# Kernel optimization log

Hardware: AMD Instinct MI355X
Metric: run time of the kernel (lower is better)

## Reference

```python
import jax, jax.numpy as jnp
import numpy as np

WEIGHT_GRADIENT = 0.05
EPS = 1e-6


def _normalize(q, eps):
    # torch F.normalize: q / max(||q||, eps)
    n = jnp.sqrt(jnp.sum(q * q, axis=1, keepdims=True))
    return q / jnp.maximum(n, eps)


def _grad_mag(q, eps):
    # depthwise conv with [-1,1] kernels == finite differences, then replicate-pad
    gx = q[..., :, 1:] - q[..., :, :-1]          # (B,4,H,W-1)
    gy = q[..., 1:, :] - q[..., :-1, :]          # (B,4,H-1,W)
    gx = jnp.pad(gx, ((0, 0), (0, 0), (0, 0), (0, 1)), mode='edge')
    gy = jnp.pad(gy, ((0, 0), (0, 0), (0, 1), (0, 0)), mode='edge')
    return jnp.sqrt(gx * gx + gy * gy + eps)


def setup_inputs() -> dict:
    key = jax.random.key(0)
    k1, k2, k3 = jax.random.split(key, 3)
    B, H, W, S = 16, 256, 256, 24
    q_pred = jax.random.normal(k1, (B, 4, H, W), dtype=jnp.float32)
    q_target = jax.random.normal(k2, (B, 4, H, W), dtype=jnp.float32)
    syms = jax.random.normal(k3, (S, 4), dtype=jnp.float32)
    syms = syms / jnp.linalg.norm(syms, axis=1, keepdims=True)  # unit quaternions
    return {"q_pred": q_pred, "q_target": q_target, "syms": syms}


def reference(q_pred, q_target, syms, eps=EPS):
    # (B,4,H,W) -> (N,4)
    qp = _normalize(q_pred.transpose(0, 2, 3, 1).reshape(-1, 4), eps)
    qt = _normalize(q_target.transpose(0, 2, 3, 1).reshape(-1, 4), eps)
    w1, x1, y1, z1 = qp[:, 0], qp[:, 1], qp[:, 2], qp[:, 3]
    w2, x2, y2, z2 = qt[:, 0], qt[:, 1], qt[:, 2], qt[:, 3]
    # relative quaternion r = qt * conj(qp)
    rw = w2 * w1 + x2 * x1 + y2 * y1 + z2 * z1
    rx = -w2 * x1 + x2 * w1 - y2 * z1 + z2 * y1
    ry = -w2 * y1 + x2 * z1 + y2 * w1 - z2 * x1
    rz = -w2 * z1 - x2 * y1 + y2 * x1 + z2 * w1
    r4 = jnp.stack([rw, rx, ry, rz], axis=1)                 # (N,4)
    signs = jnp.array([1.0, -1.0, -1.0, -1.0], dtype=syms.dtype)
    # w_dist[n,s] = rw*s_w - rx*s_x - ry*s_y - rz*s_z
    w_dist = jnp.einsum('nc,sc->ns', r4, syms * signs)       # (N,S)
    max_w = jnp.max(jnp.abs(w_dist), axis=1)
    max_w = jnp.clip(max_w, -(1.0 - eps), 1.0 - eps)
    loss_rot = jnp.mean(2.0 * jnp.arccos(max_w))
    gp = _grad_mag(q_pred, eps)
    gt = _grad_mag(q_target, eps)
    loss_grad = jnp.mean(jnp.abs(gp - gt))
    return loss_rot + WEIGHT_GRADIENT * loss_grad
```

## Files before the change

kernel.cpp:

```cpp
#include <hip/hip_runtime.h>
#include <math.h>

constexpr int Hc = 256;
constexpr int Wc = 256;
constexpr float EPSf = 1e-6f;

__device__ __forceinline__ float comp(const float4& v, int p) {
    return p == 0 ? v.x : p == 1 ? v.y : p == 2 ? v.z : v.w;
}

__device__ __forceinline__ float fast_acos01(float x) {
    float t = __builtin_amdgcn_sqrtf(1.0f - x);
    float p = fmaf(fmaf(fmaf(-0.0187293f, x, 0.0742610f), x, -0.2121144f),
                   x, 1.5707288f);
    return t * p;
}

__device__ __forceinline__ float fast_sqrt(float x) {
    return __builtin_amdgcn_sqrtf(x);
}

template<int S>
__global__ __launch_bounds__(256, 4) void sym_loss_main(
    const float* __restrict__ qp,
    const float* __restrict__ qt,
    const float* __restrict__ syms,
    float* __restrict__ out,
    float cRot, float cGrad)
{
    int t    = blockIdx.x * 256 + threadIdx.x;
    int lane = t & 63;
    int row  = t >> 6;
    int b    = row >> 8;
    int h    = row & (Hc - 1);
    int w0   = lane << 2;

    int idx0 = (b << 18) + (h << 8) + w0;
    int dy = (h == Hc - 1) ? -Wc : Wc;
    int xo = (lane == 63) ? 2 : 4;

    float4 Cp[4], Yp[4], Ct[4], Yt[4];
    float  xp[4], xt[4];
    #pragma unroll
    for (int c = 0; c < 4; ++c) {
        int idx = idx0 + (c << 16);
        Cp[c] = *(const float4*)(qp + idx);
        Yp[c] = *(const float4*)(qp + idx + dy);
        xp[c] = qp[idx + xo];
        Ct[c] = *(const float4*)(qt + idx);
        Yt[c] = *(const float4*)(qt + idx + dy);
        xt[c] = qt[idx + xo];
    }

    float gsum = 0.0f;
    #pragma unroll
    for (int c = 0; c < 4; ++c) {
        float4 C = Cp[c], Y = Yp[c], D = Ct[c], Z = Yt[c];
        float gx, gy, a, e;
        gx = C.y - C.x; gy = Y.x - C.x;
        a = fast_sqrt(fmaf(gx, gx, fmaf(gy, gy, EPSf)));
        gx = D.y - D.x; gy = Z.x - D.x;
        e = fast_sqrt(fmaf(gx, gx, fmaf(gy, gy, EPSf)));
        gsum += fabsf(a - e);

        gx = C.z - C.y; gy = Y.y - C.y;
        a = fast_sqrt(fmaf(gx, gx, fmaf(gy, gy, EPSf)));
        gx = D.z - D.y; gy = Z.y - D.y;
        e = fast_sqrt(fmaf(gx, gx, fmaf(gy, gy, EPSf)));
        gsum += fabsf(a - e);

        gx = C.w - C.z; gy = Y.z - C.z;
        a = fast_sqrt(fmaf(gx, gx, fmaf(gy, gy, EPSf)));
        gx = D.w - D.z; gy = Z.z - D.z;
        e = fast_sqrt(fmaf(gx, gx, fmaf(gy, gy, EPSf)));
        gsum += fabsf(a - e);

        gx = xp[c] - C.w; gy = Y.w - C.w;
        a = fast_sqrt(fmaf(gx, gx, fmaf(gy, gy, EPSf)));
        gx = xt[c] - D.w; gy = Z.w - D.w;
        e = fast_sqrt(fmaf(gx, gx, fmaf(gy, gy, EPSf)));
        gsum += fabsf(a - e);
    }

    float rw[4], nx[4], ny[4], nz[4];
    #pragma unroll
    for (int p = 0; p < 4; ++p) {
        float a0 = comp(Cp[0], p), a1 = comp(Cp[1], p),
              a2 = comp(Cp[2], p), a3 = comp(Cp[3], p);
        float b0 = comp(Ct[0], p), b1 = comp(Ct[1], p),
              b2 = comp(Ct[2], p), b3 = comp(Ct[3], p);

        float ss1 = fmaf(a0, a0, fmaf(a1, a1, fmaf(a2, a2, a3 * a3)));
        float ss2 = fmaf(b0, b0, fmaf(b1, b1, fmaf(b2, b2, b3 * b3)));
        float i1 = __builtin_amdgcn_rsqf(ss1);
        float i2 = __builtin_amdgcn_rsqf(ss2);
        float w1 = a0 * i1, x1 = a1 * i1, y1 = a2 * i1, z1 = a3 * i1;
        float w2 = b0 * i2, x2 = b1 * i2, y2 = b2 * i2, z2 = b3 * i2;

        rw[p] =  w2 * w1 + x2 * x1 + y2 * y1 + z2 * z1;
        float rx = -w2 * x1 + x2 * w1 - y2 * z1 + z2 * y1;
        float ry = -w2 * y1 + x2 * z1 + y2 * w1 - z2 * x1;
        float rz = -w2 * z1 - x2 * y1 + y2 * x1 + z2 * w1;
        nx[p] = -rx; ny[p] = -ry; nz[p] = -rz;
    }

    const float4* __restrict__ sv4 = (const float4*)syms;
    float maxw[4] = {0.f, 0.f, 0.f, 0.f};
    #pragma unroll
    for (int s = 0; s < S; ++s) {
        float4 sv = sv4[s];
        #pragma unroll
        for (int p = 0; p < 4; ++p) {
            float d = fmaf(nz[p], sv.w,
                      fmaf(ny[p], sv.z,
                      fmaf(nx[p], sv.y, rw[p] * sv.x)));
            maxw[p] = fmaxf(maxw[p], fabsf(d));
        }
    }
    float rot = 0.0f;
    #pragma unroll
    for (int p = 0; p < 4; ++p)
        rot += fast_acos01(fminf(maxw[p], 1.0f - EPSf));

    #pragma unroll
    for (int off = 32; off > 0; off >>= 1) {
        rot  += __shfl_down(rot,  off, 64);
        gsum += __shfl_down(gsum, off, 64);
    }
    __shared__ float s_r[4], s_g[4];
    int wid = threadIdx.x >> 6;
    if ((threadIdx.x & 63) == 0) { s_r[wid] = rot; s_g[wid] = gsum; }
    __syncthreads();
    if (threadIdx.x == 0) {
        float r = s_r[0] + s_r[1] + s_r[2] + s_r[3];
        float g = s_g[0] + s_g[1] + s_g[2] + s_g[3];
        atomicAdd(out, fmaf(r, cRot, g * cGrad));
    }
}

__global__ __launch_bounds__(256) void sym_loss_generic(
    const float* __restrict__ qp,
    const float* __restrict__ qt,
    const float* __restrict__ syms,
    int S,
    float* __restrict__ out,
    float cRot, float cGrad)
{
    int t    = blockIdx.x * 256 + threadIdx.x;
    int lane = t & 63;
    int row  = t >> 6;
    int b    = row >> 8;
    int h    = row & (Hc - 1);
    int w0   = lane << 2;
    int idx0 = (b << 18) + (h << 8) + w0;
    int dy = (h == Hc - 1) ? -Wc : Wc;
    int xo = (lane == 63) ? 2 : 4;

    float4 Cp[4], Yp[4], Ct[4], Yt[4];
    float  xp[4], xt[4];
    #pragma unroll
    for (int c = 0; c < 4; ++c) {
        int idx = idx0 + (c << 16);
        Cp[c] = *(const float4*)(qp + idx);
        Yp[c] = *(const float4*)(qp + idx + dy);
        xp[c] = qp[idx + xo];
        Ct[c] = *(const float4*)(qt + idx);
        Yt[c] = *(const float4*)(qt + idx + dy);
        xt[c] = qt[idx + xo];
    }
    float gsum = 0.0f;
    #pragma unroll
    for (int c = 0; c < 4; ++c) {
        float4 C = Cp[c], Y = Yp[c], D = Ct[c], Z = Yt[c];
        float gx, gy, a, e;
        gx = C.y - C.x; gy = Y.x - C.x;
        a = fast_sqrt(fmaf(gx, gx, fmaf(gy, gy, EPSf)));
        gx = D.y - D.x; gy = Z.x - D.x;
        e = fast_sqrt(fmaf(gx, gx, fmaf(gy, gy, EPSf)));
        gsum += fabsf(a - e);
        gx = C.z - C.y; gy = Y.y - C.y;
        a = fast_sqrt(fmaf(gx, gx, fmaf(gy, gy, EPSf)));
        gx = D.z - D.y; gy = Z.y - D.y;
        e = fast_sqrt(fmaf(gx, gx, fmaf(gy, gy, EPSf)));
        gsum += fabsf(a - e);
        gx = C.w - C.z; gy = Y.z - C.z;
        a = fast_sqrt(fmaf(gx, gx, fmaf(gy, gy, EPSf)));
        gx = D.w - D.z; gy = Z.z - D.z;
        e = fast_sqrt(fmaf(gx, gx, fmaf(gy, gy, EPSf)));
        gsum += fabsf(a - e);
        gx = xp[c] - C.w; gy = Y.w - C.w;
        a = fast_sqrt(fmaf(gx, gx, fmaf(gy, gy, EPSf)));
        gx = xt[c] - D.w; gy = Z.w - D.w;
        e = fast_sqrt(fmaf(gx, gx, fmaf(gy, gy, EPSf)));
        gsum += fabsf(a - e);
    }
    float rw[4], nx[4], ny[4], nz[4];
    #pragma unroll
    for (int p = 0; p < 4; ++p) {
        float a0 = comp(Cp[0], p), a1 = comp(Cp[1], p),
              a2 = comp(Cp[2], p), a3 = comp(Cp[3], p);
        float b0 = comp(Ct[0], p), b1 = comp(Ct[1], p),
              b2 = comp(Ct[2], p), b3 = comp(Ct[3], p);
        float ss1 = fmaf(a0, a0, fmaf(a1, a1, fmaf(a2, a2, a3 * a3)));
        float ss2 = fmaf(b0, b0, fmaf(b1, b1, fmaf(b2, b2, b3 * b3)));
        float i1 = __builtin_amdgcn_rsqf(ss1);
        float i2 = __builtin_amdgcn_rsqf(ss2);
        float w1 = a0 * i1, x1 = a1 * i1, y1 = a2 * i1, z1 = a3 * i1;
        float w2 = b0 * i2, x2 = b1 * i2, y2 = b2 * i2, z2 = b3 * i2;
        rw[p] =  w2 * w1 + x2 * x1 + y2 * y1 + z2 * z1;
        float rx = -w2 * x1 + x2 * w1 - y2 * z1 + z2 * y1;
        float ry = -w2 * y1 + x2 * z1 + y2 * w1 - z2 * x1;
        float rz = -w2 * z1 - x2 * y1 + y2 * x1 + z2 * w1;
        nx[p] = -rx; ny[p] = -ry; nz[p] = -rz;
    }
    const float4* __restrict__ sv4 = (const float4*)syms;
    float maxw[4] = {0.f, 0.f, 0.f, 0.f};
    for (int s = 0; s < S; ++s) {
        float4 sv = sv4[s];
        #pragma unroll
        for (int p = 0; p < 4; ++p) {
            float d = fmaf(nz[p], sv.w,
                      fmaf(ny[p], sv.z,
                      fmaf(nx[p], sv.y, rw[p] * sv.x)));
            maxw[p] = fmaxf(maxw[p], fabsf(d));
        }
    }
    float rot = 0.0f;
    #pragma unroll
    for (int p = 0; p < 4; ++p)
        rot += fast_acos01(fminf(maxw[p], 1.0f - EPSf));
    #pragma unroll
    for (int off = 32; off > 0; off >>= 1) {
        rot  += __shfl_down(rot,  off, 64);
        gsum += __shfl_down(gsum, off, 64);
    }
    __shared__ float s_r[4], s_g[4];
    int wid = threadIdx.x >> 6;
    if ((threadIdx.x & 63) == 0) { s_r[wid] = rot; s_g[wid] = gsum; }
    __syncthreads();
    if (threadIdx.x == 0) {
        float r = s_r[0] + s_r[1] + s_r[2] + s_r[3];
        float g = s_g[0] + s_g[1] + s_g[2] + s_g[3];
        atomicAdd(out, fmaf(r, cRot, g * cGrad));
    }
}

extern "C" void kernel_launch(void* const* d_in, const int* in_sizes, int n_in,
                              void* d_out, int out_size, void* d_ws, size_t ws_size,
                              hipStream_t stream)
{
    const float* qp   = (const float*)d_in[0];
    const float* qt   = (const float*)d_in[1];
    const float* syms = (const float*)d_in[2];
    float* out = (float*)d_out;

    int S  = in_sizes[2] / 4;
    int NP = in_sizes[0] / 4;
    int nthreads = NP / 4;
    int nblocks  = nthreads / 256;

    float cRot  = (float)(2.0 / (double)NP);
    float cGrad = (float)(0.05 / ((double)NP * 4.0));

    hipMemsetAsync(out, 0, sizeof(float), stream);

    if (S == 24) {
        sym_loss_main<24><<<nblocks, 256, 0, stream>>>(qp, qt, syms, out,
                                                       cRot, cGrad);
    } else {
        sym_loss_generic<<<nblocks, 256, 0, stream>>>(qp, qt, syms, S, out,
                                                      cRot, cGrad);
    }
}
```

Measured before the change: 90.58 us.

## Share neighbor rows via LDS and replace atomics with two-pass reduction

Each block's four wavefronts now store their loaded rows in shared memory, so the row below and the right-neighbor element are read from LDS instead of issuing extra global loads. Only the last wave loads the next row from global memory. The global atomicAdd and memset are replaced by per-block partial sums written to workspace and a separate single-block reduce kernel accumulating in double. This cuts redundant global traffic and atomic contention, at the cost of 32KB of LDS per block (which may limit occupancy), a barrier, and an extra kernel launch.

```diff
diff --git a/kernel.cpp b/kernel.cpp
--- a/kernel.cpp
+++ b/kernel.cpp
@@ -25,37 +25,59 @@
     const float* __restrict__ qp,
     const float* __restrict__ qt,
     const float* __restrict__ syms,
-    float* __restrict__ out,
-    float cRot, float cGrad)
+    float2* __restrict__ partial)
 {
-    int t    = blockIdx.x * 256 + threadIdx.x;
-    int lane = t & 63;
-    int row  = t >> 6;
+    __shared__ float lds[2 * 4 * 4 * 256];
+
+    int tid  = threadIdx.x;
+    int lane = tid & 63;
+    int wid  = tid >> 6;
+    int row  = (blockIdx.x << 2) + wid;
     int b    = row >> 8;
     int h    = row & (Hc - 1);
     int w0   = lane << 2;
 
     int idx0 = (b << 18) + (h << 8) + w0;
-    int dy = (h == Hc - 1) ? -Wc : Wc;
-    int xo = (lane == 63) ? 2 : 4;
-
-    float4 Cp[4], Yp[4], Ct[4], Yt[4];
-    float  xp[4], xt[4];
+    int dy   = (h == Hc - 1) ? -Wc : Wc;
+    int xw   = w0 + ((lane == 63) ? 2 : 4);
+
+    float4 Cp[4], Ct[4], Yp3[4], Yt3[4];
     #pragma unroll
     for (int c = 0; c < 4; ++c) {
         int idx = idx0 + (c << 16);
         Cp[c] = *(const float4*)(qp + idx);
-        Yp[c] = *(const float4*)(qp + idx + dy);
-        xp[c] = qp[idx + xo];
         Ct[c] = *(const float4*)(qt + idx);
-        Yt[c] = *(const float4*)(qt + idx + dy);
-        xt[c] = qt[idx + xo];
-    }
+    }
+    if (wid == 3) {
+        #pragma unroll
+        for (int c = 0; c < 4; ++c) {
+            int idx = idx0 + (c << 16) + dy;
+            Yp3[c] = *(const float4*)(qp + idx);
+            Yt3[c] = *(const float4*)(qt + idx);
+        }
+    }
+
+    #pragma unroll
+    for (int c = 0; c < 4; ++c) {
+        *(float4*)&lds[(((0 * 4 + c) * 4 + wid) << 8) + w0] = Cp[c];
+        *(float4*)&lds[(((1 * 4 + c) * 4 + wid) << 8) + w0] = Ct[c];
+    }
+    __syncthreads();
 
     float gsum = 0.0f;
     #pragma unroll
     for (int c = 0; c < 4; ++c) {
-        float4 C = Cp[c], Y = Yp[c], D = Ct[c], Z = Yt[c];
+        float4 C = Cp[c], D = Ct[c];
+        float4 Y, Z;
+        if (wid < 3) {
+            Y = *(const float4*)&lds[(((0 * 4 + c) * 4 + wid + 1) << 8) + w0];
+            Z = *(const float4*)&lds[(((1 * 4 + c) * 4 + wid + 1) << 8) + w0];
+        } else {
+            Y = Yp3[c]; Z = Yt3[c];
+        }
+        float xp = lds[(((0 * 4 + c) * 4 + wid) << 8) + xw];
+        float xt = lds[(((1 * 4 + c) * 4 + wid) << 8) + xw];
+
         float gx, gy, a, e;
         gx = C.y - C.x; gy = Y.x - C.x;
         a = fast_sqrt(fmaf(gx, gx, fmaf(gy, gy, EPSf)));
@@ -75,9 +97,9 @@
         e = fast_sqrt(fmaf(gx, gx, fmaf(gy, gy, EPSf)));
         gsum += fabsf(a - e);
 
-        gx = xp[c] - C.w; gy = Y.w - C.w;
-        a = fast_sqrt(fmaf(gx, gx, fmaf(gy, gy, EPSf)));
-        gx = xt[c] - D.w; gy = Z.w - D.w;
+        gx = xp - C.w;  gy = Y.w - C.w;
+        a = fast_sqrt(fmaf(gx, gx, fmaf(gy, gy, EPSf)));
+        gx = xt - D.w;  gy = Z.w - D.w;
         e = fast_sqrt(fmaf(gx, gx, fmaf(gy, gy, EPSf)));
         gsum += fabsf(a - e);
     }
@@ -128,13 +150,13 @@
         gsum += __shfl_down(gsum, off, 64);
     }
     __shared__ float s_r[4], s_g[4];
-    int wid = threadIdx.x >> 6;
-    if ((threadIdx.x & 63) == 0) { s_r[wid] = rot; s_g[wid] = gsum; }
+    if (lane == 0) { s_r[wid] = rot; s_g[wid] = gsum; }
     __syncthreads();
-    if (threadIdx.x == 0) {
-        float r = s_r[0] + s_r[1] + s_r[2] + s_r[3];
-        float g = s_g[0] + s_g[1] + s_g[2] + s_g[3];
-        atomicAdd(out, fmaf(r, cRot, g * cGrad));
+    if (tid == 0) {
+        float2 o;
+        o.x = s_r[0] + s_r[1] + s_r[2] + s_r[3];
+        o.y = s_g[0] + s_g[1] + s_g[2] + s_g[3];
+        partial[blockIdx.x] = o;
     }
 }
 
@@ -143,8 +165,7 @@
     const float* __restrict__ qt,
     const float* __restrict__ syms,
     int S,
-    float* __restrict__ out,
-    float cRot, float cGrad)
+    float2* __restrict__ partial)
 {
     int t    = blockIdx.x * 256 + threadIdx.x;
     int lane = t & 63;
@@ -239,9 +260,36 @@
     if ((threadIdx.x & 63) == 0) { s_r[wid] = rot; s_g[wid] = gsum; }
     __syncthreads();
     if (threadIdx.x == 0) {
-        float r = s_r[0] + s_r[1] + s_r[2] + s_r[3];
-        float g = s_g[0] + s_g[1] + s_g[2] + s_g[3];
-        atomicAdd(out, fmaf(r, cRot, g * cGrad));
+        float2 o;
+        o.x = s_r[0] + s_r[1] + s_r[2] + s_r[3];
+        o.y = s_g[0] + s_g[1] + s_g[2] + s_g[3];
+        partial[blockIdx.x] = o;
+    }
+}
+
+__global__ __launch_bounds__(256) void sym_loss_reduce(
+    const float2* __restrict__ partial, int nblocks,
+    float* __restrict__ out, double cRot, double cGrad)
+{
+    double r = 0.0, g = 0.0;
+    for (int i = threadIdx.x; i < nblocks; i += 256) {
+        float2 p = partial[i];
+        r += (double)p.x;
+        g += (double)p.y;
+    }
+    #pragma unroll
+    for (int off = 32; off > 0; off >>= 1) {
+        r += __shfl_down(r, off, 64);
+        g += __shfl_down(g, off, 64);
+    }
+    __shared__ double s_r[4], s_g[4];
+    int wid = threadIdx.x >> 6;
+    if ((threadIdx.x & 63) == 0) { s_r[wid] = r; s_g[wid] = g; }
+    __syncthreads();
+    if (threadIdx.x == 0) {
+        double rr = s_r[0] + s_r[1] + s_r[2] + s_r[3];
+        double gg = s_g[0] + s_g[1] + s_g[2] + s_g[3];
+        out[0] = (float)(rr * cRot + gg * cGrad);
     }
 }
 
@@ -252,23 +300,24 @@
     const float* qp   = (const float*)d_in[0];
     const float* qt   = (const float*)d_in[1];
     const float* syms = (const float*)d_in[2];
-    float* out = (float*)d_out;
 
     int S  = in_sizes[2] / 4;
     int NP = in_sizes[0] / 4;
-    int nthreads = NP / 4;
-    int nblocks  = nthreads / 256;
-
-    float cRot  = (float)(2.0 / (double)NP);
-    float cGrad = (float)(0.05 / ((double)NP * 4.0));
-
-    hipMemsetAsync(out, 0, sizeof(float), stream);
-
+
+    float2* partial = (float2*)d_ws;
+
+    double cRot  = 2.0 / (double)NP;
+    double cGrad = 0.05 / ((double)NP * 4.0);
+
+    int nblocks;
     if (S == 24) {
-        sym_loss_main<24><<<nblocks, 256, 0, stream>>>(qp, qt, syms, out,
-                                                       cRot, cGrad);
+        nblocks = NP / 1024;
+        sym_loss_main<24><<<nblocks, 256, 0, stream>>>(qp, qt, syms, partial);
     } else {
-        sym_loss_generic<<<nblocks, 256, 0, stream>>>(qp, qt, syms, S, out,
-                                                      cRot, cGrad);
-    }
-}
+        nblocks = (NP / 4) / 256;
+        sym_loss_generic<<<nblocks, 256, 0, stream>>>(qp, qt, syms, S, partial);
+    }
+
+    sym_loss_reduce<<<1, 256, 0, stream>>>(partial, nblocks, (float*)d_out,
+                                           cRot, cGrad);
+}
```

Result: no change. 88.85 us (-1.9%).
